# Kernel optimization log

Measured on AMD Instinct MI355X. Metric: run time of the kernel, lower is better.

Reference implementation:

```python
import jax, jax.numpy as jnp
import numpy as np

EPS = 1e-6


def setup_inputs() -> dict:
    key = jax.random.key(0)
    k1, k2 = jax.random.split(key)
    T, B, D, n = 2048, 16, 1024, 64
    x = jax.random.normal(k1, (T, B, D), dtype=jnp.float32)
    S0 = jnp.zeros((B, n, n), dtype=jnp.float32)
    G0 = jnp.zeros((B, n, n), dtype=jnp.float32)
    # xavier-uniform-ish init for each n x D block of the fused projection
    limit = float(np.sqrt(6.0 / (n + D)))
    W_kvqm = jax.random.uniform(k2, (4 * n, D), dtype=jnp.float32, minval=-limit, maxval=limit)
    b_s_gate = jnp.full((n,), 2.0, dtype=jnp.float32)
    b_g_gate = jnp.full((n,), 2.5, dtype=jnp.float32)
    return {"x": x, "S0": S0, "G0": G0, "W_kvqm": W_kvqm,
            "b_s_gate": b_s_gate, "b_g_gate": b_g_gate}


def _e81_forward(x, S0, G0, W_kvqm, b_s_gate, b_g_gate):
    T, B, D = x.shape
    n = b_s_gate.shape[0]
    # Fused projection: [T, B, 4n]
    proj = jnp.einsum('tbd,nd->tbn', x, W_kvqm)
    k_all, v_all, q_all, m_all = jnp.split(proj, 4, axis=-1)

    bs = b_s_gate[None, :, None]  # broadcast over [B, n(row), n(col)]
    bg = b_g_gate[None, :, None]

    def step(carry, kvqm):
        S, G = carry
        k, v, q, m_vec = kvqm  # each [B, n]
        k_norm = k / (jnp.linalg.norm(k, axis=-1, keepdims=True) + EPS)
        m_norm = m_vec / (jnp.linalg.norm(m_vec, axis=-1, keepdims=True) + EPS)

        gate_S = jax.nn.sigmoid(G + bs)
        s_retrieved = jnp.einsum('bij,bj->bi', S, k_norm)
        s_delta = v - s_retrieved
        S = gate_S * S + jnp.einsum('bi,bj->bij', s_delta, k_norm)

        gate_G = jax.nn.sigmoid(S + bg)
        g_retrieved = jnp.einsum('bij,bj->bi', G, m_norm)
        g_delta = s_delta - g_retrieved
        G = gate_G * G + jnp.einsum('bi,bj->bij', g_delta, m_norm)

        Sq = jnp.einsum('bij,bj->bi', S, q)
        out = Sq * jax.nn.silu(Sq)  # self-gated output
        return (S, G), out

    (S, G), output = jax.lax.scan(step, (S0, G0), (k_all, v_all, q_all, m_all))
    return output, S, G


def reference(x, S0, G0, W_kvqm, b_s_gate, b_g_gate):
    return _e81_forward(x, S0, G0, W_kvqm, b_s_gate, b_g_gate)
```

## Files before the change

kernel.cpp:

```cpp
#include <hip/hip_runtime.h>
#include <hip/hip_bf16.h>

#define EPS 1e-6f

typedef float f32x4 __attribute__((ext_vector_type(4)));
typedef short bf16x8 __attribute__((ext_vector_type(8)));

__device__ __forceinline__ unsigned f2bf(float x) {
  __hip_bfloat16 h = __float2bfloat16(x);
  return *reinterpret_cast<unsigned short*>(&h);
}
__device__ __forceinline__ unsigned split_pack(float x) {
  unsigned hi = f2bf(x);
  unsigned short hs = (unsigned short)hi;
  float hif = __bfloat162float(*reinterpret_cast<__hip_bfloat16*>(&hs));
  unsigned lo = f2bf(x - hif);
  return (lo << 16) | hi;
}

union FragCast { unsigned u[4]; bf16x8 v; };

constexpr int GBM = 128, GBK = 32;

__global__ __launch_bounds__(512) void proj_gemm_mfma(
    const float* __restrict__ A,
    const float* __restrict__ Bw,
    float* __restrict__ C,
    int M, int K) {
  __shared__ unsigned As[GBM * GBK];
  __shared__ unsigned Bs[256 * GBK];

  const int tid  = threadIdx.x;
  const int lane = tid & 63;
  const int wid  = tid >> 6;
  const int m0   = blockIdx.x * GBM;
  const int wm   = (wid >> 2) * 64;
  const int wn   = (wid & 3) * 64;

  const int ar = tid >> 2, ak = (tid & 3) * 8;
  const int br = tid >> 1, bk = (tid & 1) * 16;

  f32x4 acc[4][4] = {};

  for (int k0 = 0; k0 < K; k0 += GBK) {
    {
      const float* src = &A[(size_t)(m0 + ar) * K + k0 + ak];
      float4 v0 = *(const float4*)(src);
      float4 v1 = *(const float4*)(src + 4);
      unsigned p0[4] = {split_pack(v0.x), split_pack(v0.y),
                        split_pack(v0.z), split_pack(v0.w)};
      unsigned p1[4] = {split_pack(v1.x), split_pack(v1.y),
                        split_pack(v1.z), split_pack(v1.w)};
      unsigned swz  = (unsigned)(ar & 7) << 4;
      char* base = (char*)As + ar * 128;
      *(uint4*)(base + (((unsigned)ak * 4) ^ swz))       = *(uint4*)p0;
      *(uint4*)(base + (((unsigned)(ak + 4) * 4) ^ swz)) = *(uint4*)p1;
    }
    {
      const float* src = &Bw[(size_t)br * K + k0 + bk];
      unsigned swz = (unsigned)(br & 7) << 4;
      char* base = (char*)Bs + br * 128;
#pragma unroll
      for (int q = 0; q < 4; ++q) {
        float4 v = *(const float4*)(src + q * 4);
        unsigned p[4] = {split_pack(v.x), split_pack(v.y),
                         split_pack(v.z), split_pack(v.w)};
        *(uint4*)(base + (((unsigned)(bk + q * 4) * 4) ^ swz)) = *(uint4*)p;
      }
    }
    __syncthreads();

    unsigned ah[4][4], al[4][4];
    const unsigned ko = ((unsigned)(lane >> 4)) * 16;
#pragma unroll
    for (int mf = 0; mf < 4; ++mf) {
      int r = wm + mf * 16 + (lane & 15);
      unsigned swz = (unsigned)(r & 7) << 4;
      char* base = (char*)As + r * 128;
      uint4 w0 = *(uint4*)(base + (ko ^ swz));
      uint4 w1 = *(uint4*)(base + ((64 + ko) ^ swz));
      ah[mf][0] = __builtin_amdgcn_perm(w0.y, w0.x, 0x05040100);
      al[mf][0] = __builtin_amdgcn_perm(w0.y, w0.x, 0x07060302);
      ah[mf][1] = __builtin_amdgcn_perm(w0.w, w0.z, 0x05040100);
      al[mf][1] = __builtin_amdgcn_perm(w0.w, w0.z, 0x07060302);
      ah[mf][2] = __builtin_amdgcn_perm(w1.y, w1.x, 0x05040100);
      al[mf][2] = __builtin_amdgcn_perm(w1.y, w1.x, 0x07060302);
      ah[mf][3] = __builtin_amdgcn_perm(w1.w, w1.z, 0x05040100);
      al[mf][3] = __builtin_amdgcn_perm(w1.w, w1.z, 0x07060302);
    }

#pragma unroll
    for (int nf = 0; nf < 4; ++nf) {
      int r = wn + nf * 16 + (lane & 15);
      unsigned swz = (unsigned)(r & 7) << 4;
      char* base = (char*)Bs + r * 128;
      uint4 w0 = *(uint4*)(base + (ko ^ swz));
      uint4 w1 = *(uint4*)(base + ((64 + ko) ^ swz));
      FragCast bh, bl;
      bh.u[0] = __builtin_amdgcn_perm(w0.y, w0.x, 0x05040100);
      bl.u[0] = __builtin_amdgcn_perm(w0.y, w0.x, 0x07060302);
      bh.u[1] = __builtin_amdgcn_perm(w0.w, w0.z, 0x05040100);
      bl.u[1] = __builtin_amdgcn_perm(w0.w, w0.z, 0x07060302);
      bh.u[2] = __builtin_amdgcn_perm(w1.y, w1.x, 0x05040100);
      bl.u[2] = __builtin_amdgcn_perm(w1.y, w1.x, 0x07060302);
      bh.u[3] = __builtin_amdgcn_perm(w1.w, w1.z, 0x05040100);
      bl.u[3] = __builtin_amdgcn_perm(w1.w, w1.z, 0x07060302);
#pragma unroll
      for (int mf = 0; mf < 4; ++mf) {
        FragCast fah, fal;
        fah.u[0] = ah[mf][0]; fah.u[1] = ah[mf][1];
        fah.u[2] = ah[mf][2]; fah.u[3] = ah[mf][3];
        fal.u[0] = al[mf][0]; fal.u[1] = al[mf][1];
        fal.u[2] = al[mf][2]; fal.u[3] = al[mf][3];
        acc[mf][nf] = __builtin_amdgcn_mfma_f32_16x16x32_bf16(
            fah.v, bh.v, acc[mf][nf], 0, 0, 0);
        acc[mf][nf] = __builtin_amdgcn_mfma_f32_16x16x32_bf16(
            fah.v, bl.v, acc[mf][nf], 0, 0, 0);
        acc[mf][nf] = __builtin_amdgcn_mfma_f32_16x16x32_bf16(
            fal.v, bh.v, acc[mf][nf], 0, 0, 0);
      }
    }
    __syncthreads();
  }

#pragma unroll
  for (int mf = 0; mf < 4; ++mf) {
    int row = m0 + wm + mf * 16 + (lane >> 4) * 4;
#pragma unroll
    for (int nf = 0; nf < 4; ++nf) {
      int col = wn + nf * 16 + (lane & 15);
#pragma unroll
      for (int r = 0; r < 4; ++r)
        C[(size_t)(row + r) * 256 + col] = acc[mf][nf][r];
    }
  }
}

template <int CTRL>
__device__ __forceinline__ float dpp_mov(float v) {
  return __int_as_float(
      __builtin_amdgcn_update_dpp(0, __float_as_int(v), CTRL, 0xF, 0xF, true));
}

__device__ __forceinline__ float wave_sum_all(float v) {
  v += dpp_mov<0x121>(v);
  v += dpp_mov<0x122>(v);
  v += dpp_mov<0x124>(v);
  v += dpp_mov<0x128>(v);
  v += dpp_mov<0x142>(v);
  v += dpp_mov<0x143>(v);
  return __int_as_float(__builtin_amdgcn_readlane(__float_as_int(v), 63));
}

__device__ __forceinline__ float sigmoidf(float x) {
  return __builtin_amdgcn_rcpf(1.0f + __expf(-x));
}

__global__ __launch_bounds__(256) void normalize_km(float* __restrict__ proj,
                                                    int rows) {
  const int w = blockIdx.x * 4 + (threadIdx.x >> 6);
  const int lane = threadIdx.x & 63;
  if (w >= rows) return;
  float* p = proj + (size_t)w * 256;
  float k = p[lane];
  float m = p[192 + lane];
  float nk = sqrtf(wave_sum_all(k * k)) + EPS;
  float nm = sqrtf(wave_sum_all(m * m)) + EPS;
  p[lane]       = k * __builtin_amdgcn_rcpf(nk);
  p[192 + lane] = m * __builtin_amdgcn_rcpf(nm);
}

__global__ __launch_bounds__(256) void e81_scan(
    const float* __restrict__ proj,
    const float* __restrict__ S0,
    const float* __restrict__ G0,
    const float* __restrict__ bsg,
    const float* __restrict__ bgg,
    float* __restrict__ dout,
    int T) {
  const int lane = threadIdx.x & 63;
  const int wave = threadIdx.x >> 6;
  const int b    = blockIdx.x >> 4;
  const int row  = ((blockIdx.x & 15) << 2) + wave;

  const int sg_idx = (((b << 6) + row) << 6) + lane;
  float S = S0[sg_idx];
  float G = G0[sg_idx];
  const float bsi = bsg[row];
  const float bgi = bgg[row];

  float* outp = dout;
  float* Sout = dout + (size_t)T * 16 * 64;
  float* Gout = Sout + 16 * 64 * 64;

  const float* p = proj + b * 256;
  float kj = p[lane];
  float vi = p[64 + row];
  float qj = p[128 + lane];
  float mj = p[192 + lane];

  for (int t = 0; t < T; ++t) {
    const float* pn = (t + 1 < T) ? (p + 16 * 256) : p;
    float kjn = pn[lane];
    float vin = pn[64 + row];
    float qjn = pn[128 + lane];
    float mjn = pn[192 + lane];

    float sr = wave_sum_all(S * kj);
    float gr = wave_sum_all(G * mj);
    float gateS = sigmoidf(G + bsi);
    float sdelta = vi - sr;
    S = fmaf(gateS, S, sdelta * kj);
    float gateG = sigmoidf(S + bgi);
    G = fmaf(gateG, G, (sdelta - gr) * mj);

    float sq = wave_sum_all(S * qj);
    if (lane == 0)
      outp[(((size_t)t << 4) + b) * 64 + row] = sq * sq * sigmoidf(sq);

    kj = kjn; vi = vin; qj = qjn; mj = mjn;
    p = pn;
  }

  Sout[sg_idx] = S;
  Gout[sg_idx] = G;
}

extern "C" void kernel_launch(void* const* d_in, const int* in_sizes, int n_in,
                              void* d_out, int out_size, void* d_ws, size_t ws_size,
                              hipStream_t stream) {
  const float* x  = (const float*)d_in[0];
  const float* S0 = (const float*)d_in[1];
  const float* G0 = (const float*)d_in[2];
  const float* W  = (const float*)d_in[3];
  const float* bs = (const float*)d_in[4];
  const float* bg = (const float*)d_in[5];
  float* out = (float*)d_out;
  float* proj = (float*)d_ws;

  const int B = 16, D = 1024;
  const int T = in_sizes[0] / (B * D);
  const int M = T * B;

  proj_gemm_mfma<<<dim3(M / GBM), 512, 0, stream>>>(x, W, proj, M, D);

  normalize_km<<<dim3(M / 4), 256, 0, stream>>>(proj, M);

  e81_scan<<<dim3(256), 256, 0, stream>>>(proj, S0, G0, bs, bg, out, T);
}
```

Measured before the change: 934.4 us.

## Pack four matrix rows per wave with 16-lane reductions and permuted k/q/m layout

The scan kernel now handles four rows of S/G per 64-lane wave, with each lane holding four columns. This shortens each dot-product reduction from a full-wave DPP sum plus readlane to a 16-lane DPP reduction, and cuts the wave count per batch fourfold. The normalize kernel permutes the k, q and m columns so that each lane can fetch its four interleaved entries with a float4 load. The sigmoids now use exp2 with the bias pre-folded into the exponent. Each lane carries more serial work per step, which may lengthen the latency-bound recurrence.

```diff
diff --git a/kernel.cpp b/kernel.cpp
--- a/kernel.cpp
+++ b/kernel.cpp
@@ -152,8 +152,22 @@
   return __int_as_float(__builtin_amdgcn_readlane(__float_as_int(v), 63));
 }
 
-__device__ __forceinline__ float sigmoidf(float x) {
-  return __builtin_amdgcn_rcpf(1.0f + __expf(-x));
+__device__ __forceinline__ float reduce16(float v) {
+  v += dpp_mov<0x121>(v);
+  v += dpp_mov<0x122>(v);
+  v += dpp_mov<0x124>(v);
+  v += dpp_mov<0x128>(v);
+  return v;
+}
+
+#define L2E 1.4426950408889634f
+__device__ __forceinline__ float sigm_b(float x, float nb) {
+  float t = __builtin_amdgcn_exp2f(fmaf(x, -L2E, nb));
+  return __builtin_amdgcn_rcpf(1.0f + t);
+}
+__device__ __forceinline__ float sigm(float x) {
+  float t = __builtin_amdgcn_exp2f(x * -L2E);
+  return __builtin_amdgcn_rcpf(1.0f + t);
 }
 
 __global__ __launch_bounds__(256) void normalize_km(float* __restrict__ proj,
@@ -162,15 +176,18 @@
   const int lane = threadIdx.x & 63;
   if (w >= rows) return;
   float* p = proj + (size_t)w * 256;
-  float k = p[lane];
-  float m = p[192 + lane];
+  const int src = 16 * (lane & 3) + (lane >> 2);
+  float k = p[src];
+  float q = p[128 + src];
+  float m = p[192 + src];
   float nk = sqrtf(wave_sum_all(k * k)) + EPS;
   float nm = sqrtf(wave_sum_all(m * m)) + EPS;
   p[lane]       = k * __builtin_amdgcn_rcpf(nk);
+  p[128 + lane] = q;
   p[192 + lane] = m * __builtin_amdgcn_rcpf(nm);
 }
 
-__global__ __launch_bounds__(256) void e81_scan(
+__global__ __launch_bounds__(64) void e81_scan(
     const float* __restrict__ proj,
     const float* __restrict__ S0,
     const float* __restrict__ G0,
@@ -178,52 +195,81 @@
     const float* __restrict__ bgg,
     float* __restrict__ dout,
     int T) {
-  const int lane = threadIdx.x & 63;
-  const int wave = threadIdx.x >> 6;
-  const int b    = blockIdx.x >> 4;
-  const int row  = ((blockIdx.x & 15) << 2) + wave;
-
-  const int sg_idx = (((b << 6) + row) << 6) + lane;
-  float S = S0[sg_idx];
-  float G = G0[sg_idx];
-  const float bsi = bsg[row];
-  const float bgi = bgg[row];
+  const int lane = threadIdx.x;
+  const int l = lane & 15;
+  const int g = lane >> 4;
+  const int b  = blockIdx.x >> 4;
+  const int wb = blockIdx.x & 15;
+  const int row = wb * 4 + g;
+
+  const size_t sgbase = ((size_t)(b * 64 + row)) * 64 + l;
+  float S[4], G[4];
+#pragma unroll
+  for (int e = 0; e < 4; ++e) {
+    S[e] = S0[sgbase + 16 * e];
+    G[e] = G0[sgbase + 16 * e];
+  }
+  const float nbs = -bsg[row] * L2E;
+  const float nbg = -bgg[row] * L2E;
 
   float* outp = dout;
   float* Sout = dout + (size_t)T * 16 * 64;
   float* Gout = Sout + 16 * 64 * 64;
 
   const float* p = proj + b * 256;
-  float kj = p[lane];
-  float vi = p[64 + row];
-  float qj = p[128 + lane];
-  float mj = p[192 + lane];
+  float4 k = *(const float4*)(p + 4 * l);
+  float4 q = *(const float4*)(p + 128 + 4 * l);
+  float4 m = *(const float4*)(p + 192 + 4 * l);
+  float  v = p[64 + row];
 
   for (int t = 0; t < T; ++t) {
     const float* pn = (t + 1 < T) ? (p + 16 * 256) : p;
-    float kjn = pn[lane];
-    float vin = pn[64 + row];
-    float qjn = pn[128 + lane];
-    float mjn = pn[192 + lane];
-
-    float sr = wave_sum_all(S * kj);
-    float gr = wave_sum_all(G * mj);
-    float gateS = sigmoidf(G + bsi);
-    float sdelta = vi - sr;
-    S = fmaf(gateS, S, sdelta * kj);
-    float gateG = sigmoidf(S + bgi);
-    G = fmaf(gateG, G, (sdelta - gr) * mj);
-
-    float sq = wave_sum_all(S * qj);
-    if (lane == 0)
-      outp[(((size_t)t << 4) + b) * 64 + row] = sq * sq * sigmoidf(sq);
-
-    kj = kjn; vi = vin; qj = qjn; mj = mjn;
+    float4 kn = *(const float4*)(pn + 4 * l);
+    float4 qn = *(const float4*)(pn + 128 + 4 * l);
+    float4 mn = *(const float4*)(pn + 192 + 4 * l);
+    float  vn = pn[64 + row];
+
+    float sr = S[0] * k.x;
+    sr = fmaf(S[1], k.y, sr);
+    sr = fmaf(S[2], k.z, sr);
+    sr = fmaf(S[3], k.w, sr);
+    sr = reduce16(sr);
+    float gr = G[0] * m.x;
+    gr = fmaf(G[1], m.y, gr);
+    gr = fmaf(G[2], m.z, gr);
+    gr = fmaf(G[3], m.w, gr);
+    gr = reduce16(gr);
+
+    float sdelta = v - sr;
+    S[0] = fmaf(sigm_b(G[0], nbs), S[0], sdelta * k.x);
+    S[1] = fmaf(sigm_b(G[1], nbs), S[1], sdelta * k.y);
+    S[2] = fmaf(sigm_b(G[2], nbs), S[2], sdelta * k.z);
+    S[3] = fmaf(sigm_b(G[3], nbs), S[3], sdelta * k.w);
+
+    float gd = sdelta - gr;
+    G[0] = fmaf(sigm_b(S[0], nbg), G[0], gd * m.x);
+    G[1] = fmaf(sigm_b(S[1], nbg), G[1], gd * m.y);
+    G[2] = fmaf(sigm_b(S[2], nbg), G[2], gd * m.z);
+    G[3] = fmaf(sigm_b(S[3], nbg), G[3], gd * m.w);
+
+    float sq = S[0] * q.x;
+    sq = fmaf(S[1], q.y, sq);
+    sq = fmaf(S[2], q.z, sq);
+    sq = fmaf(S[3], q.w, sq);
+    sq = reduce16(sq);
+
+    if (l == 0)
+      outp[(((size_t)t << 4) + b) * 64 + row] = sq * sq * sigm(sq);
+
+    k = kn; q = qn; m = mn; v = vn;
     p = pn;
   }
 
-  Sout[sg_idx] = S;
-  Gout[sg_idx] = G;
+#pragma unroll
+  for (int e = 0; e < 4; ++e) {
+    Sout[sgbase + 16 * e] = S[e];
+    Gout[sgbase + 16 * e] = G[e];
+  }
 }
 
 extern "C" void kernel_launch(void* const* d_in, const int* in_sizes, int n_in,
@@ -246,5 +292,5 @@
 
   normalize_km<<<dim3(M / 4), 256, 0, stream>>>(proj, M);
 
-  e81_scan<<<dim3(256), 256, 0, stream>>>(proj, S0, G0, bs, bg, out, T);
-}
+  e81_scan<<<dim3(256), 64, 0, stream>>>(proj, S0, G0, bs, bg, out, T);
+}
```

Result: faster. 885.5 us (-5.2%).
